# Performance work log

Hardware: AMD Instinct MI355X
Metric: run time of the kernel (lower is better)

## Reference

```python
import jax, jax.numpy as jnp
from jax import lax
import numpy as np

DN = ('NCHW', 'OIHW', 'NCHW')


def _conv(x, w, b):
    y = lax.conv_general_dilated(x, w, (1, 1), 'SAME', dimension_numbers=DN)
    return y + b[None, :, None, None]


def setup_inputs() -> dict:
    key = jax.random.key(0)
    ks = jax.random.split(key, 8)
    B = 2
    noise = 0.1 * jax.random.normal(ks[0], (B, 768, 577), dtype=jnp.float32)  # N(0, 0.1)
    targets = jax.random.randint(ks[1], (B, 384, 384), 0, 171)
    w1 = 0.02 * jax.random.normal(ks[2], (512, 768, 3, 3), dtype=jnp.float32)
    b1 = 0.02 * jax.random.normal(ks[3], (512,), dtype=jnp.float32)
    w2 = 0.02 * jax.random.normal(ks[4], (512, 512, 3, 3), dtype=jnp.float32)
    b2 = 0.02 * jax.random.normal(ks[5], (512,), dtype=jnp.float32)
    w3 = 0.2 * jax.random.normal(ks[6], (77,), dtype=jnp.float32)  # Con3: Conv2d(1,77,1x1)
    b3 = 0.2 * jax.random.normal(ks[7], (77,), dtype=jnp.float32)
    return {'noise': noise, 'targets': targets, 'w1': w1, 'b1': b1,
            'w2': w2, 'b2': b2, 'w3': w3, 'b3': b3}


def reference(noise, targets, w1, b1, w2, b2, w3, b3):
    B = noise.shape[0]
    # NoiseToImage is shadowed by an empty nn.Sequential() -> identity
    image_noise = jnp.transpose(noise, (2, 0, 1))  # (577, B, 768)

    # --- NoiseToText ---
    H, W = targets.shape[1], targets.shape[2]
    ih = (jnp.arange(24) * H) // 24  # nearest-neighbor interpolate indices
    iw = (jnp.arange(24) * W) // 24
    m = targets[:, ih][:, :, iw]  # (B, 24, 24) class labels
    # one-hot scatter into 256 channels, keep first 171 (labels >=171 -> all-zero)
    mask = (m[:, None] == jnp.arange(171)[None, :, None, None]).astype(noise.dtype)  # (B,171,24,24)

    x = noise[:, :, 1:].reshape(B, 768, 24, 24)  # drop CLS token
    xm = x[:, None] * mask[:, :, None]            # (B,171,768,24,24)
    xm = xm.reshape(B * 171, 768, 24, 24)

    y = _conv(xm, w1, b1)                         # (B*171,512,24,24)
    y = y.reshape(-1, 512, 6, 4, 6, 4).mean(axis=(3, 5))  # AdaptiveAvgPool2d((6,6))
    y = _conv(y, w2, b2)                          # (B*171,512,6,6)
    y = y.mean(axis=(2, 3))                       # AdaptiveAvgPool2d((1,1)) -> (B*171,512)
    y = y.reshape(B, 171, 1, 512).transpose(0, 2, 1, 3)  # (B,1,171,512)
    # Con3: 1x1 conv with in_channels=1, out_channels=77
    text_noise = w3[None, :, None, None] * y + b3[None, :, None, None]  # (B,77,171,512)
    return image_noise, text_noise
```

## Files before the change

kernel.cpp:

```cpp
#include <hip/hip_runtime.h>
#include <hip/hip_bf16.h>

typedef unsigned short u16;
typedef short bf16x8 __attribute__((ext_vector_type(8)));
typedef float f32x4 __attribute__((ext_vector_type(4)));

__device__ __forceinline__ u16 f2bf(float f){
    unsigned u = __float_as_uint(f);
    unsigned r = 0x7fffu + ((u >> 16) & 1u);
    return (u16)((u + r) >> 16);
}

__device__ __forceinline__ void gload_lds16(const u16* g, u16* lds_base){
    __builtin_amdgcn_global_load_lds(
        (const __attribute__((address_space(1))) unsigned int*)g,
        (__attribute__((address_space(3))) unsigned int*)lds_base, 16, 0, 0);
}

#define OUT0_N 886272
#define OUT1_N 13483008
#define YN 175104
#define KS2 12

__global__ void k_prep(const float* __restrict__ noise, const int* __restrict__ targets,
                       const float* __restrict__ w1, const float* __restrict__ b1,
                       const float* __restrict__ w2, const float* __restrict__ b2,
                       float* __restrict__ out0, u16* __restrict__ XbfT,
                       u16* __restrict__ Are, u16* __restrict__ Mfull16,
                       float* __restrict__ bias, int* __restrict__ labels,
                       u16* __restrict__ Zcat16){
    __shared__ float sh[32 * 33];
    int blk = blockIdx.x;
    int tid = threadIdx.x;
    if (blk < 912){
        int b   = blk / 456;
        int rem = blk % 456;
        int cb  = rem / 19, sb = rem % 19;
        int tx = tid & 31, ty = tid >> 5;
        int s0 = sb * 32, c0 = cb * 32;
        float (*tile)[33] = (float(*)[33])sh;
        #pragma unroll
        for (int i = 0; i < 4; i++){
            int c = c0 + ty + i * 8;
            int s = s0 + tx;
            if (s < 577) tile[ty + i * 8][tx] = noise[(size_t)(b * 768 + c) * 577 + s];
        }
        __syncthreads();
        #pragma unroll
        for (int i = 0; i < 4; i++){
            int s = s0 + ty + i * 8;
            int c = c0 + tx;
            if (s >= 577) continue;
            float v = tile[tx][ty + i * 8];
            out0[(size_t)(s * 2 + b) * 768 + c] = v;
            if (s >= 1) XbfT[(size_t)(b * 576 + s - 1) * 768 + c] = f2bf(v);
        }
    } else if (blk < 2448){
        int idx = (blk - 912) * 256 + tid;
        int k = idx % 768; int c1 = idx / 768;
        const float* wp = w1 + (size_t)idx * 9;
        #pragma unroll
        for (int tap = 0; tap < 9; tap++)
            Are[(size_t)(c1 * 9 + tap) * 768 + k] = f2bf(wp[tap]);
    } else if (blk < 3472){
        int idx = (blk - 2448) * 256 + tid;
        int c1 = idx % 512, c2 = idx / 512;
        const float* wp = w2 + (size_t)(c2 * 512 + c1) * 9;
        float t[3][3];
        #pragma unroll
        for (int r = 0; r < 3; r++)
            #pragma unroll
            for (int s = 0; s < 3; s++)
                t[r][s] = wp[r * 3 + s];
        float cs0[3], cs1[3], cs2[3];
        #pragma unroll
        for (int r = 0; r < 3; r++){
            cs0[r] = t[r][0] + t[r][1];
            cs1[r] = t[r][0] + t[r][1] + t[r][2];
            cs2[r] = t[r][1] + t[r][2];
        }
        const float inv = 1.0f / 576.0f;
        u16* Mp = Mfull16 + (size_t)(c2 * 512 + c1) * 9;
        Mp[0] = f2bf(inv * (cs0[0] + cs0[1]));
        Mp[1] = f2bf(inv * (cs1[0] + cs1[1]));
        Mp[2] = f2bf(inv * (cs2[0] + cs2[1]));
        Mp[3] = f2bf(inv * (cs0[0] + cs0[1] + cs0[2]));
        Mp[4] = f2bf(inv * (cs1[0] + cs1[1] + cs1[2]));
        Mp[5] = f2bf(inv * (cs2[0] + cs2[1] + cs2[2]));
        Mp[6] = f2bf(inv * (cs0[1] + cs0[2]));
        Mp[7] = f2bf(inv * (cs1[1] + cs1[2]));
        Mp[8] = f2bf(inv * (cs2[1] + cs2[2]));
    } else if (blk < 3984){
        int c2 = blk - 3472;
        const float cw[9] = {25.f,30.f,25.f,30.f,36.f,30.f,25.f,30.f,25.f};
        float sb = 0.f;
        for (int c1 = tid; c1 < 512; c1 += 256){
            const float* wp = w2 + (size_t)(c2 * 512 + c1) * 9;
            float s = 0.f;
            #pragma unroll
            for (int q = 0; q < 9; q++) s += wp[q] * cw[q];
            sb += b1[c1] * s;
        }
        sh[tid] = sb; __syncthreads();
        for (int o = 128; o > 0; o >>= 1){ if (tid < o) sh[tid] += sh[tid + o]; __syncthreads(); }
        if (tid == 0) bias[c2] = b2[c2] + sh[0] * (1.0f / 36.0f);
    } else if (blk < 3989){
        int idx = (blk - 3984) * 256 + tid;
        if (idx < 1152){
            int b = idx / 576; int p = idx % 576;
            int i = p / 24, j = p % 24;
            labels[idx] = targets[b * 147456 + i * 16 * 384 + j * 16];
        }
    } else {
        int idx = (blk - 3989) * 256 + tid;
        if (idx < 193536) Zcat16[342 * 4608 + idx] = 0;
    }
}

__launch_bounds__(256)
__global__ void k_gemm1(const u16* __restrict__ Are, const u16* __restrict__ XbfT,
                        float* __restrict__ D){
    __shared__ u16 As[128 * 64];
    __shared__ u16 Bs[64 * 64];
    int tid  = threadIdx.x;
    int wave = tid >> 6, lane = tid & 63;
    int l16 = lane & 15, quad = lane >> 4;
    int wm = wave >> 1, wn = wave & 1;
    int m0 = blockIdx.x * 128;
    int n0 = blockIdx.y * 64;
    int srow = lane >> 3, scol = (lane & 7) * 8;
    f32x4 acc[4][2] = {};
    for (int k0 = 0; k0 < 768; k0 += 64){
        #pragma unroll
        for (int j = 0; j < 4; j++){
            int ch = wave * 4 + j;
            gload_lds16(Are + (size_t)(m0 + ch * 8 + srow) * 768 + k0 + scol, &As[ch * 512]);
        }
        #pragma unroll
        for (int j = 0; j < 2; j++){
            int ch = wave * 2 + j;
            gload_lds16(XbfT + (size_t)(n0 + ch * 8 + srow) * 768 + k0 + scol, &Bs[ch * 512]);
        }
        __syncthreads();
        #pragma unroll
        for (int ks = 0; ks < 2; ks++){
            bf16x8 af[4], bf[2];
            #pragma unroll
            for (int i = 0; i < 4; i++)
                af[i] = *(const bf16x8*)&As[(wm * 64 + i * 16 + l16) * 64 + ks * 32 + quad * 8];
            #pragma unroll
            for (int i = 0; i < 2; i++)
                bf[i] = *(const bf16x8*)&Bs[(wn * 32 + i * 16 + l16) * 64 + ks * 32 + quad * 8];
            #pragma unroll
            for (int mi = 0; mi < 4; mi++)
                #pragma unroll
                for (int ni = 0; ni < 2; ni++)
                    acc[mi][ni] = __builtin_amdgcn_mfma_f32_16x16x32_bf16(af[mi], bf[ni], acc[mi][ni], 0, 0, 0);
        }
        __syncthreads();
    }
    #pragma unroll
    for (int mi = 0; mi < 4; mi++)
        #pragma unroll
        for (int ni = 0; ni < 2; ni++)
            #pragma unroll
            for (int r = 0; r < 4; r++)
                D[(size_t)(m0 + wm * 64 + mi * 16 + quad * 4 + r) * 1152 + n0 + wn * 32 + ni * 16 + l16] = acc[mi][ni][r];
}

__launch_bounds__(256)
__global__ void k_scatter(const float* __restrict__ D, const int* __restrict__ labels,
                          u16* __restrict__ Zcat16){
    int blk = blockIdx.x;
    int b  = blk >> 9;
    int c1 = blk & 511;
    __shared__ float acc[171 * 9];
    int t = threadIdx.x;
    for (int q = t; q < 1539; q += 256) acc[q] = 0.f;
    __syncthreads();
    for (int p = t; p < 576; p += 256){
        int cls = labels[b * 576 + p];
        if (cls < 0 || cls >= 171) continue;
        int i = p / 24, j = p % 24;
        float slot[9];
        #pragma unroll
        for (int q = 0; q < 9; q++) slot[q] = 0.f;
        unsigned used = 0;
        int tau[3]; bool vs[3];
        #pragma unroll
        for (int s1 = 0; s1 < 3; s1++){
            int v = j - s1 + 1;
            vs[s1]  = (v >= 0 && v < 24);
            tau[s1] = (v < 4) ? 0 : ((v < 20) ? 1 : 2);
        }
        #pragma unroll
        for (int r1 = 0; r1 < 3; r1++){
            int u = i - r1 + 1;
            if (u < 0 || u >= 24) continue;
            int rho = (u < 4) ? 0 : ((u < 20) ? 1 : 2);
            #pragma unroll
            for (int s1 = 0; s1 < 3; s1++){
                if (!vs[s1]) continue;
                float tv = D[(size_t)(c1 * 9 + r1 * 3 + s1) * 1152 + b * 576 + p];
                int sl = rho * 3 + tau[s1];
                slot[sl] += tv;
                used |= 1u << sl;
            }
        }
        #pragma unroll
        for (int sl = 0; sl < 9; sl++)
            if (used & (1u << sl)) atomicAdd(&acc[cls * 9 + sl], slot[sl]);
    }
    __syncthreads();
    for (int q = t; q < 1539; q += 256){
        int cls = q / 9, sl = q % 9;
        Zcat16[(size_t)(b * 171 + cls) * 4608 + c1 * 9 + sl] = f2bf(acc[q]);
    }
}

__launch_bounds__(256)
__global__ void k_gemm2m(const u16* __restrict__ Zcat16, const u16* __restrict__ Mfull16,
                         float* __restrict__ ypart){
    __shared__ u16 As[128 * 64];
    __shared__ u16 Bs[64 * 64];
    int tid  = threadIdx.x;
    int wave = tid >> 6, lane = tid & 63;
    int l16 = lane & 15, quad = lane >> 4;
    int wm = wave >> 1, wn = wave & 1;
    int m0 = blockIdx.x * 128;
    int n0 = blockIdx.y * 64;
    int kbeg = blockIdx.z * 384;
    int srow = lane >> 3, scol = (lane & 7) * 8;
    f32x4 acc[4][2] = {};
    for (int k0 = kbeg; k0 < kbeg + 384; k0 += 64){
        #pragma unroll
        for (int j = 0; j < 4; j++){
            int ch = wave * 4 + j;
            gload_lds16(Zcat16 + (size_t)(m0 + ch * 8 + srow) * 4608 + k0 + scol, &As[ch * 512]);
        }
        #pragma unroll
        for (int j = 0; j < 2; j++){
            int ch = wave * 2 + j;
            gload_lds16(Mfull16 + (size_t)(n0 + ch * 8 + srow) * 4608 + k0 + scol, &Bs[ch * 512]);
        }
        __syncthreads();
        #pragma unroll
        for (int ks = 0; ks < 2; ks++){
            bf16x8 af[4], bf[2];
            #pragma unroll
            for (int i = 0; i < 4; i++)
                af[i] = *(const bf16x8*)&As[(wm * 64 + i * 16 + l16) * 64 + ks * 32 + quad * 8];
            #pragma unroll
            for (int i = 0; i < 2; i++)
                bf[i] = *(const bf16x8*)&Bs[(wn * 32 + i * 16 + l16) * 64 + ks * 32 + quad * 8];
            #pragma unroll
            for (int mi = 0; mi < 4; mi++)
                #pragma unroll
                for (int ni = 0; ni < 2; ni++)
                    acc[mi][ni] = __builtin_amdgcn_mfma_f32_16x16x32_bf16(af[mi], bf[ni], acc[mi][ni], 0, 0, 0);
        }
        __syncthreads();
    }
    float* yp = ypart + (size_t)blockIdx.z * YN;
    #pragma unroll
    for (int mi = 0; mi < 4; mi++)
        #pragma unroll
        for (int r = 0; r < 4; r++){
            int n = m0 + wm * 64 + mi * 16 + quad * 4 + r;
            if (n >= 342) continue;
            #pragma unroll
            for (int ni = 0; ni < 2; ni++)
                yp[(size_t)n * 512 + n0 + wn * 32 + ni * 16 + l16] = acc[mi][ni][r];
        }
}

__global__ void k_red(const float* __restrict__ ypart, const float* __restrict__ bias,
                      float4* __restrict__ ysum){
    int idx = blockIdx.x * 128 + threadIdx.x;
    int c4 = idx & 127;
    int n  = idx >> 7;
    float4 sum = ((const float4*)bias)[c4];
    #pragma unroll
    for (int s = 0; s < KS2; s++){
        float4 v = *(const float4*)&ypart[(size_t)s * YN + (size_t)n * 512 + c4 * 4];
        sum.x += v.x; sum.y += v.y; sum.z += v.z; sum.w += v.w;
    }
    ysum[idx] = sum;
}

__global__ void k_expand(const float4* __restrict__ ysum, const float* __restrict__ w3,
                         const float* __restrict__ b3, float4* __restrict__ out1){
    int idx = blockIdx.x * 256 + threadIdx.x;
    if (idx >= OUT1_N / 4) return;
    int c4 = idx & 127;
    int t  = idx >> 7;
    int cls = t % 171;
    int u   = t / 171;
    int o   = u % 77;
    int b   = u / 77;
    float w  = w3[o];
    float bb = b3[o];
    float4 v = ysum[(b * 171 + cls) * 128 + c4];
    out1[idx] = make_float4(w * v.x + bb, w * v.y + bb, w * v.z + bb, w * v.w + bb);
}

extern "C" void kernel_launch(void* const* d_in, const int* in_sizes, int n_in,
                              void* d_out, int out_size, void* d_ws, size_t ws_size,
                              hipStream_t stream) {
    const float* noise   = (const float*)d_in[0];
    const int*   targets = (const int*)  d_in[1];
    const float* w1      = (const float*)d_in[2];
    const float* b1      = (const float*)d_in[3];
    const float* w2      = (const float*)d_in[4];
    const float* b2      = (const float*)d_in[5];
    const float* w3      = (const float*)d_in[6];
    const float* b3      = (const float*)d_in[7];
    float* out0 = (float*)d_out;
    float* out1 = out0 + OUT0_N;

    char* ws = (char*)d_ws;
    const size_t OFF_ARE  = 0;
    const size_t OFF_X    = 7077888;
    const size_t OFF_D    = OFF_X   + 1769472;
    const size_t OFF_MF   = OFF_D   + 21233664;
    const size_t OFF_ZC   = OFF_MF  + 4718592;
    const size_t OFF_BIAS = OFF_ZC  + 3538944;
    const size_t OFF_LAB  = OFF_BIAS + 2048;
    const size_t OFF_YS   = OFF_LAB + 4608;

    u16*   Are    = (u16*)  (ws + OFF_ARE);
    u16*   XbfT   = (u16*)  (ws + OFF_X);
    float* D      = (float*)(ws + OFF_D);
    float* ypart  = (float*)(ws + OFF_D);
    u16*   Mfull16= (u16*)  (ws + OFF_MF);
    u16*   Zcat16 = (u16*)  (ws + OFF_ZC);
    float* bias   = (float*)(ws + OFF_BIAS);
    int*   labels = (int*)  (ws + OFF_LAB);
    float* ysum   = (float*)(ws + OFF_YS);

    k_prep  <<<4745, 256, 0, stream>>>(noise, targets, w1, b1, w2, b2,
                                       out0, XbfT, Are, Mfull16, bias, labels, Zcat16);
    k_gemm1 <<<dim3(36, 18), 256, 0, stream>>>(Are, XbfT, D);
    k_scatter<<<1024, 256, 0, stream>>>(D, labels, Zcat16);
    k_gemm2m<<<dim3(3, 8, KS2), 256, 0, stream>>>(Zcat16, Mfull16, ypart);
    k_red   <<<342, 128, 0, stream>>>(ypart, bias, (float4*)ysum);
    k_expand<<<13167, 256, 0, stream>>>((const float4*)ysum, w3, b3, (float4*)out1);
}
```

Measured before the change: 158.4 us.

## Fuse bias reduction into w2 prep blocks and retile gemm1 to 96x128

```diff
diff --git a/kernel.cpp b/kernel.cpp
--- a/kernel.cpp
+++ b/kernel.cpp
@@ -24,10 +24,10 @@
 
 __global__ void k_prep(const float* __restrict__ noise, const int* __restrict__ targets,
                        const float* __restrict__ w1, const float* __restrict__ b1,
-                       const float* __restrict__ w2, const float* __restrict__ b2,
+                       const float* __restrict__ w2,
                        float* __restrict__ out0, u16* __restrict__ XbfT,
                        u16* __restrict__ Are, u16* __restrict__ Mfull16,
-                       float* __restrict__ bias, int* __restrict__ labels,
+                       float* __restrict__ biasH, int* __restrict__ labels,
                        u16* __restrict__ Zcat16){
     __shared__ float sh[32 * 33];
     int blk = blockIdx.x;
@@ -63,8 +63,9 @@
         for (int tap = 0; tap < 9; tap++)
             Are[(size_t)(c1 * 9 + tap) * 768 + k] = f2bf(wp[tap]);
     } else if (blk < 3472){
-        int idx = (blk - 2448) * 256 + tid;
-        int c1 = idx % 512, c2 = idx / 512;
+        int b2i = blk - 2448;
+        int c2 = b2i >> 1, h = b2i & 1;
+        int c1 = h * 256 + tid;
         const float* wp = w2 + (size_t)(c2 * 512 + c1) * 9;
         float t[3][3];
         #pragma unroll
@@ -90,29 +91,22 @@
         Mp[6] = f2bf(inv * (cs0[1] + cs0[2]));
         Mp[7] = f2bf(inv * (cs1[1] + cs1[2]));
         Mp[8] = f2bf(inv * (cs2[1] + cs2[2]));
-    } else if (blk < 3984){
-        int c2 = blk - 3472;
-        const float cw[9] = {25.f,30.f,25.f,30.f,36.f,30.f,25.f,30.f,25.f};
-        float sb = 0.f;
-        for (int c1 = tid; c1 < 512; c1 += 256){
-            const float* wp = w2 + (size_t)(c2 * 512 + c1) * 9;
-            float s = 0.f;
-            #pragma unroll
-            for (int q = 0; q < 9; q++) s += wp[q] * cw[q];
-            sb += b1[c1] * s;
-        }
-        sh[tid] = sb; __syncthreads();
+        float s_cw = 25.f * (t[0][0] + t[0][2] + t[2][0] + t[2][2])
+                   + 30.f * (t[0][1] + t[1][0] + t[1][2] + t[2][1])
+                   + 36.f * t[1][1];
+        sh[tid] = b1[c1] * s_cw;
+        __syncthreads();
         for (int o = 128; o > 0; o >>= 1){ if (tid < o) sh[tid] += sh[tid + o]; __syncthreads(); }
-        if (tid == 0) bias[c2] = b2[c2] + sh[0] * (1.0f / 36.0f);
-    } else if (blk < 3989){
-        int idx = (blk - 3984) * 256 + tid;
+        if (tid == 0) biasH[h * 512 + c2] = sh[0] * (1.0f / 36.0f);
+    } else if (blk < 3477){
+        int idx = (blk - 3472) * 256 + tid;
         if (idx < 1152){
             int b = idx / 576; int p = idx % 576;
             int i = p / 24, j = p % 24;
             labels[idx] = targets[b * 147456 + i * 16 * 384 + j * 16];
         }
     } else {
-        int idx = (blk - 3989) * 256 + tid;
+        int idx = (blk - 3477) * 256 + tid;
         if (idx < 193536) Zcat16[342 * 4608 + idx] = 0;
     }
 }
@@ -120,52 +114,52 @@
 __launch_bounds__(256)
 __global__ void k_gemm1(const u16* __restrict__ Are, const u16* __restrict__ XbfT,
                         float* __restrict__ D){
-    __shared__ u16 As[128 * 64];
-    __shared__ u16 Bs[64 * 64];
+    __shared__ u16 As[96 * 64];
+    __shared__ u16 Bs[128 * 64];
     int tid  = threadIdx.x;
     int wave = tid >> 6, lane = tid & 63;
     int l16 = lane & 15, quad = lane >> 4;
     int wm = wave >> 1, wn = wave & 1;
-    int m0 = blockIdx.x * 128;
-    int n0 = blockIdx.y * 64;
+    int m0 = blockIdx.x * 96;
+    int n0 = blockIdx.y * 128;
     int srow = lane >> 3, scol = (lane & 7) * 8;
-    f32x4 acc[4][2] = {};
+    f32x4 acc[3][4] = {};
     for (int k0 = 0; k0 < 768; k0 += 64){
+        #pragma unroll
+        for (int j = 0; j < 3; j++){
+            int ch = wave * 3 + j;
+            gload_lds16(Are + (size_t)(m0 + ch * 8 + srow) * 768 + k0 + scol, &As[ch * 512]);
+        }
         #pragma unroll
         for (int j = 0; j < 4; j++){
             int ch = wave * 4 + j;
-            gload_lds16(Are + (size_t)(m0 + ch * 8 + srow) * 768 + k0 + scol, &As[ch * 512]);
-        }
-        #pragma unroll
-        for (int j = 0; j < 2; j++){
-            int ch = wave * 2 + j;
             gload_lds16(XbfT + (size_t)(n0 + ch * 8 + srow) * 768 + k0 + scol, &Bs[ch * 512]);
         }
         __syncthreads();
         #pragma unroll
         for (int ks = 0; ks < 2; ks++){
-            bf16x8 af[4], bf[2];
+            bf16x8 af[3], bf[4];
+            #pragma unroll
+            for (int i = 0; i < 3; i++)
+                af[i] = *(const bf16x8*)&As[(wm * 48 + i * 16 + l16) * 64 + ks * 32 + quad * 8];
             #pragma unroll
             for (int i = 0; i < 4; i++)
-                af[i] = *(const bf16x8*)&As[(wm * 64 + i * 16 + l16) * 64 + ks * 32 + quad * 8];
-            #pragma unroll
-            for (int i = 0; i < 2; i++)
-                bf[i] = *(const bf16x8*)&Bs[(wn * 32 + i * 16 + l16) * 64 + ks * 32 + quad * 8];
-            #pragma unroll
-            for (int mi = 0; mi < 4; mi++)
+                bf[i] = *(const bf16x8*)&Bs[(wn * 64 + i * 16 + l16) * 64 + ks * 32 + quad * 8];
+            #pragma unroll
+            for (int mi = 0; mi < 3; mi++)
                 #pragma unroll
-                for (int ni = 0; ni < 2; ni++)
+                for (int ni = 0; ni < 4; ni++)
                     acc[mi][ni] = __builtin_amdgcn_mfma_f32_16x16x32_bf16(af[mi], bf[ni], acc[mi][ni], 0, 0, 0);
         }
         __syncthreads();
     }
     #pragma unroll
-    for (int mi = 0; mi < 4; mi++)
-        #pragma unroll
-        for (int ni = 0; ni < 2; ni++)
+    for (int mi = 0; mi < 3; mi++)
+        #pragma unroll
+        for (int ni = 0; ni < 4; ni++)
             #pragma unroll
             for (int r = 0; r < 4; r++)
-                D[(size_t)(m0 + wm * 64 + mi * 16 + quad * 4 + r) * 1152 + n0 + wn * 32 + ni * 16 + l16] = acc[mi][ni][r];
+                D[(size_t)(m0 + wm * 48 + mi * 16 + quad * 4 + r) * 1152 + n0 + wn * 64 + ni * 16 + l16] = acc[mi][ni][r];
 }
 
 __launch_bounds__(256)
@@ -274,12 +268,15 @@
         }
 }
 
-__global__ void k_red(const float* __restrict__ ypart, const float* __restrict__ bias,
-                      float4* __restrict__ ysum){
+__global__ void k_red(const float* __restrict__ ypart, const float* __restrict__ biasH,
+                      const float* __restrict__ b2, float4* __restrict__ ysum){
     int idx = blockIdx.x * 128 + threadIdx.x;
     int c4 = idx & 127;
     int n  = idx >> 7;
-    float4 sum = ((const float4*)bias)[c4];
+    float4 sum = ((const float4*)b2)[c4];
+    float4 ba  = ((const float4*)biasH)[c4];
+    float4 bb  = ((const float4*)biasH)[128 + c4];
+    sum.x += ba.x + bb.x; sum.y += ba.y + bb.y; sum.z += ba.z + bb.z; sum.w += ba.w + bb.w;
     #pragma unroll
     for (int s = 0; s < KS2; s++){
         float4 v = *(const float4*)&ypart[(size_t)s * YN + (size_t)n * 512 + c4 * 4];
@@ -324,8 +321,8 @@
     const size_t OFF_D    = OFF_X   + 1769472;
     const size_t OFF_MF   = OFF_D   + 21233664;
     const size_t OFF_ZC   = OFF_MF  + 4718592;
-    const size_t OFF_BIAS = OFF_ZC  + 3538944;
-    const size_t OFF_LAB  = OFF_BIAS + 2048;
+    const size_t OFF_BH   = OFF_ZC  + 3538944;
+    const size_t OFF_LAB  = OFF_BH  + 4096;
     const size_t OFF_YS   = OFF_LAB + 4608;
 
     u16*   Are    = (u16*)  (ws + OFF_ARE);
@@ -334,15 +331,15 @@
     float* ypart  = (float*)(ws + OFF_D);
     u16*   Mfull16= (u16*)  (ws + OFF_MF);
     u16*   Zcat16 = (u16*)  (ws + OFF_ZC);
-    float* bias   = (float*)(ws + OFF_BIAS);
+    float* biasH  = (float*)(ws + OFF_BH);
     int*   labels = (int*)  (ws + OFF_LAB);
     float* ysum   = (float*)(ws + OFF_YS);
 
-    k_prep  <<<4745, 256, 0, stream>>>(noise, targets, w1, b1, w2, b2,
-                                       out0, XbfT, Are, Mfull16, bias, labels, Zcat16);
-    k_gemm1 <<<dim3(36, 18), 256, 0, stream>>>(Are, XbfT, D);
+    k_prep  <<<4233, 256, 0, stream>>>(noise, targets, w1, b1, w2,
+                                       out0, XbfT, Are, Mfull16, biasH, labels, Zcat16);
+    k_gemm1 <<<dim3(48, 9), 256, 0, stream>>>(Are, XbfT, D);
     k_scatter<<<1024, 256, 0, stream>>>(D, labels, Zcat16);
     k_gemm2m<<<dim3(3, 8, KS2), 256, 0, stream>>>(Zcat16, Mfull16, ypart);
-    k_red   <<<342, 128, 0, stream>>>(ypart, bias, (float4*)ysum);
+    k_red   <<<342, 128, 0, stream>>>(ypart, biasH, b2, (float4*)ysum);
     k_expand<<<13167, 256, 0, stream>>>((const float4*)ysum, w3, b3, (float4*)out1);
 }
```

After: 156.8 us. About the same (-1.0%).
